# Performance work log

Measured on AMD Instinct MI355X. Metric: run time of the kernel, lower is better.

## Reference

```python
import jax, jax.numpy as jnp
import numpy as np

N_NODES = 1_000_000
DIM = 256
NUM_SEGMENTS = 8192


def setup_inputs() -> dict:
    key = jax.random.key(0)
    k1, k2, k3 = jax.random.split(key, 3)
    x = jax.random.normal(k1, (N_NODES, DIM), dtype=jnp.float32)
    batch = jnp.sort(jax.random.randint(k2, (N_NODES,), 0, NUM_SEGMENTS, dtype=jnp.int64))
    # Xavier-uniform init for Linear(dim, 1): bound = sqrt(6/(dim+1))
    bound = np.sqrt(6.0 / (DIM + 1))
    W = jax.random.uniform(k3, (1, DIM), dtype=jnp.float32, minval=-bound, maxval=bound)
    b = jnp.zeros((1,), dtype=jnp.float32)
    return {"x": x, "batch": batch, "W": W, "b": b}


def reference(x, batch, W, b):
    # gate: sigmoid(x @ W^T + b) -> [N, 1]
    score = jax.nn.sigmoid(x @ W.T + b)
    # segment-sum of gated features and segment-max of raw features -> [G, D] each
    out1 = jax.ops.segment_sum(score * x, batch, num_segments=NUM_SEGMENTS)
    out2 = jax.ops.segment_max(x, batch, num_segments=NUM_SEGMENTS)
    return jnp.concatenate([out1, out2], axis=1)  # [G, 2D]
```

## Files before the change

### kernel.cpp

```cpp
#include <hip/hip_runtime.h>
#include <math.h>

#define DIM 256
#define NSEG 8192

template <int CTRL>
__device__ __forceinline__ float dpp_add(float v) {
    int t = __builtin_amdgcn_update_dpp(0, __float_as_int(v), CTRL, 0xf, 0xf, true);
    return v + __int_as_float(t);
}
__device__ __forceinline__ float wave64_sum_bcast(float v) {
    v = dpp_add<0x111>(v);
    v = dpp_add<0x112>(v);
    v = dpp_add<0x114>(v);
    v = dpp_add<0x118>(v);
    v = dpp_add<0x142>(v);
    v = dpp_add<0x143>(v);
    return __int_as_float(__builtin_amdgcn_readlane(__float_as_int(v), 63));
}

__global__ void seg_offsets_kernel(const int* __restrict__ batch, int n,
                                   int* __restrict__ offs) {
    int i = blockIdx.x * blockDim.x + threadIdx.x;
    if (i >= n) return;
    int b    = batch[i];
    int prev = (i == 0) ? -1 : batch[i - 1];
    for (int g = prev + 1; g <= b; ++g) offs[g] = i;
    if (i == n - 1)
        for (int g = b + 1; g <= NSEG; ++g) offs[g] = n;
}

__global__ __launch_bounds__(256) void readout_seg_kernel(
    const float* __restrict__ x,
    const int*   __restrict__ batch,
    const float* __restrict__ W,
    const float* __restrict__ bvec,
    const int*   __restrict__ offs,
    float*       __restrict__ out,
    int n)
{
    const int g = blockIdx.x;

    int start, end;
    if (offs) {
        start = offs[g];
        end   = offs[g + 1];
    } else {
        int lo = 0, hi = n;
        while (lo < hi) { int m = (lo + hi) >> 1; if (batch[m] < g) lo = m + 1; else hi = m; }
        start = lo; hi = n;
        while (lo < hi) { int m = (lo + hi) >> 1; if (batch[m] < g + 1) lo = m + 1; else hi = m; }
        end = lo;
    }
    const int len = end - start;

    const int tid  = threadIdx.x;
    const int wave = tid >> 6;
    const int lane = tid & 63;

    const int wbeg = start + (int)(((long long)len * wave) >> 2);
    const int wend = start + (int)(((long long)len * (wave + 1)) >> 2);

    const float4 w4  = reinterpret_cast<const float4*>(W)[lane];
    const float bias = bvec[0];
    const float NLOG2E = -1.44269504088896f;

    float4 acc_s = make_float4(0.f, 0.f, 0.f, 0.f);
    float4 acc_m = make_float4(-INFINITY, -INFINITY, -INFINITY, -INFINITY);

    const float4* __restrict__ X4 = reinterpret_cast<const float4*>(x);

    int r = wbeg;
    for (; r + 3 < wend; r += 4) {
        const float4 v0 = X4[(long long)(r + 0) * 64 + lane];
        const float4 v1 = X4[(long long)(r + 1) * 64 + lane];
        const float4 v2 = X4[(long long)(r + 2) * 64 + lane];
        const float4 v3 = X4[(long long)(r + 3) * 64 + lane];

        float d0 = v0.x * w4.x + v0.y * w4.y + v0.z * w4.z + v0.w * w4.w;
        float d1 = v1.x * w4.x + v1.y * w4.y + v1.z * w4.z + v1.w * w4.w;
        float d2 = v2.x * w4.x + v2.y * w4.y + v2.z * w4.z + v2.w * w4.w;
        float d3 = v3.x * w4.x + v3.y * w4.y + v3.z * w4.z + v3.w * w4.w;

        d0 = wave64_sum_bcast(d0);
        d1 = wave64_sum_bcast(d1);
        d2 = wave64_sum_bcast(d2);
        d3 = wave64_sum_bcast(d3);

        const float s0 = __builtin_amdgcn_rcpf(
            1.0f + __builtin_amdgcn_exp2f((d0 + bias) * NLOG2E));
        const float s1 = __builtin_amdgcn_rcpf(
            1.0f + __builtin_amdgcn_exp2f((d1 + bias) * NLOG2E));
        const float s2 = __builtin_amdgcn_rcpf(
            1.0f + __builtin_amdgcn_exp2f((d2 + bias) * NLOG2E));
        const float s3 = __builtin_amdgcn_rcpf(
            1.0f + __builtin_amdgcn_exp2f((d3 + bias) * NLOG2E));

        acc_s.x = fmaf(s0, v0.x, acc_s.x); acc_s.y = fmaf(s0, v0.y, acc_s.y);
        acc_s.z = fmaf(s0, v0.z, acc_s.z); acc_s.w = fmaf(s0, v0.w, acc_s.w);
        acc_s.x = fmaf(s1, v1.x, acc_s.x); acc_s.y = fmaf(s1, v1.y, acc_s.y);
        acc_s.z = fmaf(s1, v1.z, acc_s.z); acc_s.w = fmaf(s1, v1.w, acc_s.w);
        acc_s.x = fmaf(s2, v2.x, acc_s.x); acc_s.y = fmaf(s2, v2.y, acc_s.y);
        acc_s.z = fmaf(s2, v2.z, acc_s.z); acc_s.w = fmaf(s2, v2.w, acc_s.w);
        acc_s.x = fmaf(s3, v3.x, acc_s.x); acc_s.y = fmaf(s3, v3.y, acc_s.y);
        acc_s.z = fmaf(s3, v3.z, acc_s.z); acc_s.w = fmaf(s3, v3.w, acc_s.w);

        acc_m.x = fmaxf(acc_m.x, fmaxf(fmaxf(v0.x, v1.x), fmaxf(v2.x, v3.x)));
        acc_m.y = fmaxf(acc_m.y, fmaxf(fmaxf(v0.y, v1.y), fmaxf(v2.y, v3.y)));
        acc_m.z = fmaxf(acc_m.z, fmaxf(fmaxf(v0.z, v1.z), fmaxf(v2.z, v3.z)));
        acc_m.w = fmaxf(acc_m.w, fmaxf(fmaxf(v0.w, v1.w), fmaxf(v2.w, v3.w)));
    }

    for (; r < wend; ++r) {
        const float4 v = X4[(long long)r * 64 + lane];
        float d = v.x * w4.x + v.y * w4.y + v.z * w4.z + v.w * w4.w;
        d = wave64_sum_bcast(d);
        const float s = __builtin_amdgcn_rcpf(
            1.0f + __builtin_amdgcn_exp2f((d + bias) * NLOG2E));
        acc_s.x = fmaf(s, v.x, acc_s.x); acc_s.y = fmaf(s, v.y, acc_s.y);
        acc_s.z = fmaf(s, v.z, acc_s.z); acc_s.w = fmaf(s, v.w, acc_s.w);
        acc_m.x = fmaxf(acc_m.x, v.x);   acc_m.y = fmaxf(acc_m.y, v.y);
        acc_m.z = fmaxf(acc_m.z, v.z);   acc_m.w = fmaxf(acc_m.w, v.w);
    }

    __shared__ float4 sm_s[4][64];
    __shared__ float4 sm_m[4][64];
    sm_s[wave][lane] = acc_s;
    sm_m[wave][lane] = acc_m;
    __syncthreads();

    if (wave == 0) {
        float4 S = sm_s[0][lane];
        float4 M = sm_m[0][lane];
        #pragma unroll
        for (int w2 = 1; w2 < 4; ++w2) {
            float4 s2 = sm_s[w2][lane];
            float4 m2 = sm_m[w2][lane];
            S.x += s2.x; S.y += s2.y; S.z += s2.z; S.w += s2.w;
            M.x = fmaxf(M.x, m2.x); M.y = fmaxf(M.y, m2.y);
            M.z = fmaxf(M.z, m2.z); M.w = fmaxf(M.w, m2.w);
        }
        float* row = out + (long long)g * (2 * DIM);
        reinterpret_cast<float4*>(row)[lane]       = S;
        reinterpret_cast<float4*>(row + DIM)[lane] = M;
    }
}

extern "C" void kernel_launch(void* const* d_in, const int* in_sizes, int n_in,
                              void* d_out, int out_size, void* d_ws, size_t ws_size,
                              hipStream_t stream) {
    const float* x     = (const float*)d_in[0];
    const int*   batch = (const int*)d_in[1];
    const float* W     = (const float*)d_in[2];
    const float* b     = (const float*)d_in[3];
    float* out = (float*)d_out;
    const int n = in_sizes[0] / DIM;

    int* offs = nullptr;
    if (ws_size >= (size_t)(NSEG + 1) * sizeof(int)) {
        offs = (int*)d_ws;
        seg_offsets_kernel<<<(n + 255) / 256, 256, 0, stream>>>(batch, n, offs);
    }
    readout_seg_kernel<<<NSEG, 256, 0, stream>>>(x, batch, W, b, offs, out, n);
}
```

Measured before the change: 194.8 us.

## Interleave rows across waves, use nontemporal loads, drop binary-search fallback

```diff
diff --git a/kernel.cpp b/kernel.cpp
--- a/kernel.cpp
+++ b/kernel.cpp
@@ -3,6 +3,8 @@
 
 #define DIM 256
 #define NSEG 8192
+
+typedef float fx4 __attribute__((ext_vector_type(4)));
 
 template <int CTRL>
 __device__ __forceinline__ float dpp_add(float v) {
@@ -32,87 +34,57 @@
 
 __global__ __launch_bounds__(256) void readout_seg_kernel(
     const float* __restrict__ x,
-    const int*   __restrict__ batch,
     const float* __restrict__ W,
     const float* __restrict__ bvec,
     const int*   __restrict__ offs,
-    float*       __restrict__ out,
-    int n)
+    float*       __restrict__ out)
 {
     const int g = blockIdx.x;
-
-    int start, end;
-    if (offs) {
-        start = offs[g];
-        end   = offs[g + 1];
-    } else {
-        int lo = 0, hi = n;
-        while (lo < hi) { int m = (lo + hi) >> 1; if (batch[m] < g) lo = m + 1; else hi = m; }
-        start = lo; hi = n;
-        while (lo < hi) { int m = (lo + hi) >> 1; if (batch[m] < g + 1) lo = m + 1; else hi = m; }
-        end = lo;
-    }
-    const int len = end - start;
+    const int start = offs[g];
+    const int end   = offs[g + 1];
 
     const int tid  = threadIdx.x;
     const int wave = tid >> 6;
     const int lane = tid & 63;
 
-    const int wbeg = start + (int)(((long long)len * wave) >> 2);
-    const int wend = start + (int)(((long long)len * (wave + 1)) >> 2);
-
-    const float4 w4  = reinterpret_cast<const float4*>(W)[lane];
+    const fx4 w4   = reinterpret_cast<const fx4*>(W)[lane];
     const float bias = bvec[0];
     const float NLOG2E = -1.44269504088896f;
 
-    float4 acc_s = make_float4(0.f, 0.f, 0.f, 0.f);
-    float4 acc_m = make_float4(-INFINITY, -INFINITY, -INFINITY, -INFINITY);
+    fx4 acc_s = (fx4){0.f, 0.f, 0.f, 0.f};
+    fx4 acc_m = (fx4){-INFINITY, -INFINITY, -INFINITY, -INFINITY};
 
-    const float4* __restrict__ X4 = reinterpret_cast<const float4*>(x);
+    const fx4* __restrict__ X4 = reinterpret_cast<const fx4*>(x);
 
-    int r = wbeg;
-    for (; r + 3 < wend; r += 4) {
-        const float4 v0 = X4[(long long)(r + 0) * 64 + lane];
-        const float4 v1 = X4[(long long)(r + 1) * 64 + lane];
-        const float4 v2 = X4[(long long)(r + 2) * 64 + lane];
-        const float4 v3 = X4[(long long)(r + 3) * 64 + lane];
+    int r = start + wave;
+    for (; r + 4 < end; r += 8) {
+        const fx4 v0 = __builtin_nontemporal_load(&X4[(long long)r * 64 + lane]);
+        const fx4 v1 = __builtin_nontemporal_load(&X4[(long long)(r + 4) * 64 + lane]);
 
         float d0 = v0.x * w4.x + v0.y * w4.y + v0.z * w4.z + v0.w * w4.w;
         float d1 = v1.x * w4.x + v1.y * w4.y + v1.z * w4.z + v1.w * w4.w;
-        float d2 = v2.x * w4.x + v2.y * w4.y + v2.z * w4.z + v2.w * w4.w;
-        float d3 = v3.x * w4.x + v3.y * w4.y + v3.z * w4.z + v3.w * w4.w;
 
         d0 = wave64_sum_bcast(d0);
         d1 = wave64_sum_bcast(d1);
-        d2 = wave64_sum_bcast(d2);
-        d3 = wave64_sum_bcast(d3);
 
         const float s0 = __builtin_amdgcn_rcpf(
             1.0f + __builtin_amdgcn_exp2f((d0 + bias) * NLOG2E));
         const float s1 = __builtin_amdgcn_rcpf(
             1.0f + __builtin_amdgcn_exp2f((d1 + bias) * NLOG2E));
-        const float s2 = __builtin_amdgcn_rcpf(
-            1.0f + __builtin_amdgcn_exp2f((d2 + bias) * NLOG2E));
-        const float s3 = __builtin_amdgcn_rcpf(
-            1.0f + __builtin_amdgcn_exp2f((d3 + bias) * NLOG2E));
 
         acc_s.x = fmaf(s0, v0.x, acc_s.x); acc_s.y = fmaf(s0, v0.y, acc_s.y);
         acc_s.z = fmaf(s0, v0.z, acc_s.z); acc_s.w = fmaf(s0, v0.w, acc_s.w);
         acc_s.x = fmaf(s1, v1.x, acc_s.x); acc_s.y = fmaf(s1, v1.y, acc_s.y);
         acc_s.z = fmaf(s1, v1.z, acc_s.z); acc_s.w = fmaf(s1, v1.w, acc_s.w);
-        acc_s.x = fmaf(s2, v2.x, acc_s.x); acc_s.y = fmaf(s2, v2.y, acc_s.y);
-        acc_s.z = fmaf(s2, v2.z, acc_s.z); acc_s.w = fmaf(s2, v2.w, acc_s.w);
-        acc_s.x = fmaf(s3, v3.x, acc_s.x); acc_s.y = fmaf(s3, v3.y, acc_s.y);
-        acc_s.z = fmaf(s3, v3.z, acc_s.z); acc_s.w = fmaf(s3, v3.w, acc_s.w);
 
-        acc_m.x = fmaxf(acc_m.x, fmaxf(fmaxf(v0.x, v1.x), fmaxf(v2.x, v3.x)));
-        acc_m.y = fmaxf(acc_m.y, fmaxf(fmaxf(v0.y, v1.y), fmaxf(v2.y, v3.y)));
-        acc_m.z = fmaxf(acc_m.z, fmaxf(fmaxf(v0.z, v1.z), fmaxf(v2.z, v3.z)));
-        acc_m.w = fmaxf(acc_m.w, fmaxf(fmaxf(v0.w, v1.w), fmaxf(v2.w, v3.w)));
+        acc_m.x = fmaxf(acc_m.x, fmaxf(v0.x, v1.x));
+        acc_m.y = fmaxf(acc_m.y, fmaxf(v0.y, v1.y));
+        acc_m.z = fmaxf(acc_m.z, fmaxf(v0.z, v1.z));
+        acc_m.w = fmaxf(acc_m.w, fmaxf(v0.w, v1.w));
     }
 
-    for (; r < wend; ++r) {
-        const float4 v = X4[(long long)r * 64 + lane];
+    if (r < end) {
+        const fx4 v = __builtin_nontemporal_load(&X4[(long long)r * 64 + lane]);
         float d = v.x * w4.x + v.y * w4.y + v.z * w4.z + v.w * w4.w;
         d = wave64_sum_bcast(d);
         const float s = __builtin_amdgcn_rcpf(
@@ -123,26 +95,26 @@
         acc_m.z = fmaxf(acc_m.z, v.z);   acc_m.w = fmaxf(acc_m.w, v.w);
     }
 
-    __shared__ float4 sm_s[4][64];
-    __shared__ float4 sm_m[4][64];
+    __shared__ fx4 sm_s[4][64];
+    __shared__ fx4 sm_m[4][64];
     sm_s[wave][lane] = acc_s;
     sm_m[wave][lane] = acc_m;
     __syncthreads();
 
     if (wave == 0) {
-        float4 S = sm_s[0][lane];
-        float4 M = sm_m[0][lane];
+        fx4 S = sm_s[0][lane];
+        fx4 M = sm_m[0][lane];
         #pragma unroll
         for (int w2 = 1; w2 < 4; ++w2) {
-            float4 s2 = sm_s[w2][lane];
-            float4 m2 = sm_m[w2][lane];
+            fx4 s2 = sm_s[w2][lane];
+            fx4 m2 = sm_m[w2][lane];
             S.x += s2.x; S.y += s2.y; S.z += s2.z; S.w += s2.w;
             M.x = fmaxf(M.x, m2.x); M.y = fmaxf(M.y, m2.y);
             M.z = fmaxf(M.z, m2.z); M.w = fmaxf(M.w, m2.w);
         }
         float* row = out + (long long)g * (2 * DIM);
-        reinterpret_cast<float4*>(row)[lane]       = S;
-        reinterpret_cast<float4*>(row + DIM)[lane] = M;
+        reinterpret_cast<fx4*>(row)[lane]       = S;
+        reinterpret_cast<fx4*>(row + DIM)[lane] = M;
     }
 }
 
@@ -156,10 +128,7 @@
     float* out = (float*)d_out;
     const int n = in_sizes[0] / DIM;
 
-    int* offs = nullptr;
-    if (ws_size >= (size_t)(NSEG + 1) * sizeof(int)) {
-        offs = (int*)d_ws;
-        seg_offsets_kernel<<<(n + 255) / 256, 256, 0, stream>>>(batch, n, offs);
-    }
-    readout_seg_kernel<<<NSEG, 256, 0, stream>>>(x, batch, W, b, offs, out, n);
+    int* offs = (int*)d_ws;
+    seg_offsets_kernel<<<(n + 255) / 256, 256, 0, stream>>>(batch, n, offs);
+    readout_seg_kernel<<<NSEG, 256, 0, stream>>>(x, W, b, offs, out);
 }
```

Result: faster. 180.9 us (-7.1%).
